# Kernel tuning notes

Measured on AMD Instinct MI355X. Metric: run time of the kernel, lower is better.

## Reference

```python
import jax, jax.numpy as jnp
import numpy as np

EPS = 1e-12  # tf.math.l2_normalize default epsilon

def _l2_normalize(x, axis):
    sq = jnp.sum(x * x, axis=axis, keepdims=True)
    return x * jax.lax.rsqrt(jnp.maximum(sq, EPS))

def setup_inputs() -> dict:
    key = jax.random.key(0)
    k1, k2 = jax.random.split(key)
    B, L, D, K = 4096, 200, 64, 8
    inputs = jax.random.normal(k1, (B, L, D), dtype=jnp.float32)
    prototype = jax.random.normal(k2, (K, D), dtype=jnp.float32)
    return {"inputs": inputs, "prototype": prototype}

def reference(inputs, prototype):
    # inputs: [B, L, D], prototype: [K, D]
    normed_interests = _l2_normalize(inputs, axis=-1)      # [B, L, D]
    normed_prototype = _l2_normalize(prototype, axis=-1)   # [K, D]
    # cosine_sim: [B, K, L] = prototype @ interests^T (broadcast over batch)
    cosine_sim = jnp.einsum('kd,bld->bkl', normed_prototype, normed_interests)
    # softmax over the slot/prototype axis K (axis=-2)
    attn = jax.nn.softmax(cosine_sim, axis=-2)              # [B, K, L]
    # projected interests: [B, K, D]
    return jnp.einsum('bkl,bld->bkd', attn, inputs)
```

## Files before the change

### kernel.cpp

```cpp
#include <hip/hip_runtime.h>


#define LQ 200
#define DQ 64
#define KQ 8
#define NSTEP 25

__device__ __forceinline__ float dppx1(float v) {
    return __int_as_float(__builtin_amdgcn_update_dpp(0, __float_as_int(v), 0xB1, 0xF, 0xF, true));
}
__device__ __forceinline__ float dppx2(float v) {
    return __int_as_float(__builtin_amdgcn_update_dpp(0, __float_as_int(v), 0x4E, 0xF, 0xF, true));
}
__device__ __forceinline__ float swz4(float v) {
    return __int_as_float(__builtin_amdgcn_ds_swizzle(__float_as_int(v), 0x101F));
}
__device__ __forceinline__ float allred8(float v) {
    v += dppx1(v); v += dppx2(v); v += swz4(v); return v;
}
__device__ __forceinline__ float dot4f(float4 a, float4 b) {
    return a.x * b.x + a.y * b.y + a.z * b.z + a.w * b.w;
}
__device__ __forceinline__ void fma4(float4& acc, float a, float4 v) {
    acc.x += a * v.x; acc.y += a * v.y; acc.z += a * v.z; acc.w += a * v.w;
}

__device__ __forceinline__ float reduce_dots(const float* s, bool b1, bool b2, bool b3) {
    float T0 = (b1 ? s[1] : s[0]) + dppx1(b1 ? s[0] : s[1]);
    float T1 = (b1 ? s[3] : s[2]) + dppx1(b1 ? s[2] : s[3]);
    float T2 = (b1 ? s[5] : s[4]) + dppx1(b1 ? s[4] : s[5]);
    float T3 = (b1 ? s[7] : s[6]) + dppx1(b1 ? s[6] : s[7]);
    float K0 = (b2 ? T1 : T0) + dppx2(b2 ? T0 : T1);
    float K1 = (b2 ? T3 : T2) + dppx2(b2 ? T2 : T3);
    return (b3 ? K1 : K0) + swz4(b3 ? K0 : K1);
}

__global__ __launch_bounds__(64, 3) void projector_kernel(const float* __restrict__ x,
                                                          const float* __restrict__ proto,
                                                          float* __restrict__ out) {
    __shared__ __align__(16) float xL[8 * DQ];
    __shared__ __align__(16) float aL[8 * KQ];

    const int b = blockIdx.x;
    const int t = threadIdx.x;
    const int c  = t & 7;
    const int r8 = t >> 3;
    const bool b1 = (c & 1) != 0;
    const bool b2 = (c & 2) != 0;
    const bool b3 = (c & 4) != 0;

    const float4* p4  = (const float4*)proto;
    const float4* xb4 = (const float4*)(x + (size_t)b * (LQ * DQ));

    float4 pA[KQ], pB[KQ];
    #pragma unroll
    for (int k = 0; k < KQ; ++k) {
        pA[k] = p4[k * 16 + 2 * c];
        pB[k] = p4[k * 16 + 2 * c + 1];
    }
    float rnp;
    {
        float sp[KQ];
        #pragma unroll
        for (int k = 0; k < KQ; ++k) sp[k] = dot4f(pA[k], pA[k]) + dot4f(pB[k], pB[k]);
        rnp = __builtin_amdgcn_rsqf(fmaxf(reduce_dots(sp, b1, b2, b3), 1e-12f));
    }

    float4 acc0 = make_float4(0.f, 0.f, 0.f, 0.f), acc1 = acc0;

    float4 xA = xb4[r8 * 16 + 2 * c], xB = xb4[r8 * 16 + 2 * c + 1];

    #pragma unroll 1
    for (int it = 0; it < NSTEP; ++it) {
        const int nr = (it + 1 < NSTEP ? (it + 1) * 8 : (NSTEP - 1) * 8) + r8;
        float4 nA = xb4[nr * 16 + 2 * c];
        float4 nB = xb4[nr * 16 + 2 * c + 1];

        float s[KQ];
        #pragma unroll
        for (int k = 0; k < KQ; ++k)
            s[k] = dot4f(xA, pA[k]) + dot4f(xB, pB[k]);
        float d  = reduce_dots(s, b1, b2, b3) * rnp;
        float sq = allred8(dot4f(xA, xA) + dot4f(xB, xB));
        float e  = __expf(d * __builtin_amdgcn_rsqf(fmaxf(sq, 1e-12f)));
        float a  = e * __builtin_amdgcn_rcpf(allred8(e));

        ((float4*)xL)[r8 * 16 + 2 * c]     = xA;
        ((float4*)xL)[r8 * 16 + 2 * c + 1] = xB;
        aL[t] = a;

        #pragma unroll
        for (int r = 0; r < 8; ++r) {
            float  av  = aL[r * KQ + r8];
            float4 xv0 = ((const float4*)xL)[r * 16 + 2 * c];
            float4 xv1 = ((const float4*)xL)[r * 16 + 2 * c + 1];
            fma4(acc0, av, xv0);
            fma4(acc1, av, xv1);
        }

        xA = nA; xB = nB;
    }

    float4* og = (float4*)(out + (size_t)b * (KQ * DQ));
    og[r8 * 16 + 2 * c]     = acc0;
    og[r8 * 16 + 2 * c + 1] = acc1;
}

extern "C" void kernel_launch(void* const* d_in, const int* in_sizes, int n_in,
                              void* d_out, int out_size, void* d_ws, size_t ws_size,
                              hipStream_t stream) {
    const float* x     = (const float*)d_in[0];
    const float* proto = (const float*)d_in[1];
    float* out = (float*)d_out;

    const int Bn = in_sizes[0] / (LQ * DQ);

    projector_kernel<<<Bn, 64, 0, stream>>>(x, proto, out);
}
```

Baseline: 43.94 us.

## Keep per-prototype accumulators in registers and reduce across rows with shuffles

Removes the per-iteration LDS staging of x rows and attention weights. Each thread now broadcasts the 8 softmax numerators within its octet via DPP/swizzle and accumulates all K prototypes for its own row slice in 64 registers. A butterfly shuffle reduction across row groups at the end assembles the outputs. Packed v2f FMAs are used for the dot products. This trades LDS traffic and barriers for much higher register pressure, and the occupancy hint in launch bounds is dropped.

```diff
diff --git a/kernel.cpp b/kernel.cpp
--- a/kernel.cpp
+++ b/kernel.cpp
@@ -5,6 +5,8 @@
 #define DQ 64
 #define KQ 8
 #define NSTEP 25
+
+typedef float v2f __attribute__((ext_vector_type(2)));
 
 __device__ __forceinline__ float dppx1(float v) {
     return __int_as_float(__builtin_amdgcn_update_dpp(0, __float_as_int(v), 0xB1, 0xF, 0xF, true));
@@ -18,12 +20,10 @@
 __device__ __forceinline__ float allred8(float v) {
     v += dppx1(v); v += dppx2(v); v += swz4(v); return v;
 }
-__device__ __forceinline__ float dot4f(float4 a, float4 b) {
-    return a.x * b.x + a.y * b.y + a.z * b.z + a.w * b.w;
+__device__ __forceinline__ v2f fma2(v2f a, v2f b, v2f c) {
+    return __builtin_elementwise_fma(a, b, c);
 }
-__device__ __forceinline__ void fma4(float4& acc, float a, float4 v) {
-    acc.x += a * v.x; acc.y += a * v.y; acc.z += a * v.z; acc.w += a * v.w;
-}
+__device__ __forceinline__ float hsum2(v2f v) { return v.x + v.y; }
 
 __device__ __forceinline__ float reduce_dots(const float* s, bool b1, bool b2, bool b3) {
     float T0 = (b1 ? s[1] : s[0]) + dppx1(b1 ? s[0] : s[1]);
@@ -35,16 +35,13 @@
     return (b3 ? K1 : K0) + swz4(b3 ? K0 : K1);
 }
 
-__global__ __launch_bounds__(64, 3) void projector_kernel(const float* __restrict__ x,
-                                                          const float* __restrict__ proto,
-                                                          float* __restrict__ out) {
-    __shared__ __align__(16) float xL[8 * DQ];
-    __shared__ __align__(16) float aL[8 * KQ];
-
+__global__ __launch_bounds__(64) void projector_kernel(const float* __restrict__ x,
+                                                       const float* __restrict__ proto,
+                                                       float* __restrict__ out) {
     const int b = blockIdx.x;
     const int t = threadIdx.x;
-    const int c  = t & 7;
-    const int r8 = t >> 3;
+    const int c = t & 7;
+    const int a = t >> 3;
     const bool b1 = (c & 1) != 0;
     const bool b2 = (c & 2) != 0;
     const bool b3 = (c & 4) != 0;
@@ -62,48 +59,100 @@
     {
         float sp[KQ];
         #pragma unroll
-        for (int k = 0; k < KQ; ++k) sp[k] = dot4f(pA[k], pA[k]) + dot4f(pB[k], pB[k]);
+        for (int k = 0; k < KQ; ++k) {
+            v2f a0 = {pA[k].x, pA[k].y}, a1 = {pA[k].z, pA[k].w};
+            v2f b0 = {pB[k].x, pB[k].y}, b1v = {pB[k].z, pB[k].w};
+            v2f t2 = fma2(b1v, b1v, fma2(b0, b0, fma2(a1, a1, a0 * a0)));
+            sp[k] = hsum2(t2);
+        }
         rnp = __builtin_amdgcn_rsqf(fmaxf(reduce_dots(sp, b1, b2, b3), 1e-12f));
     }
 
-    float4 acc0 = make_float4(0.f, 0.f, 0.f, 0.f), acc1 = acc0;
+    v2f acc[KQ][4];
+    #pragma unroll
+    for (int j = 0; j < KQ; ++j)
+        #pragma unroll
+        for (int q = 0; q < 4; ++q) acc[j][q] = (v2f){0.f, 0.f};
 
-    float4 xA = xb4[r8 * 16 + 2 * c], xB = xb4[r8 * 16 + 2 * c + 1];
+    float4 f0 = xb4[a * 16 + 2 * c], f1 = xb4[a * 16 + 2 * c + 1];
 
     #pragma unroll 1
     for (int it = 0; it < NSTEP; ++it) {
-        const int nr = (it + 1 < NSTEP ? (it + 1) * 8 : (NSTEP - 1) * 8) + r8;
-        float4 nA = xb4[nr * 16 + 2 * c];
-        float4 nB = xb4[nr * 16 + 2 * c + 1];
+        const int nrow = (it + 1 < NSTEP ? (it + 1) * 8 : (NSTEP - 1) * 8) + a;
+        float4 nf0 = xb4[nrow * 16 + 2 * c];
+        float4 nf1 = xb4[nrow * 16 + 2 * c + 1];
+
+        v2f x0 = {f0.x, f0.y}, x1 = {f0.z, f0.w};
+        v2f x2 = {f1.x, f1.y}, x3 = {f1.z, f1.w};
 
         float s[KQ];
         #pragma unroll
-        for (int k = 0; k < KQ; ++k)
-            s[k] = dot4f(xA, pA[k]) + dot4f(xB, pB[k]);
-        float d  = reduce_dots(s, b1, b2, b3) * rnp;
-        float sq = allred8(dot4f(xA, xA) + dot4f(xB, xB));
-        float e  = __expf(d * __builtin_amdgcn_rsqf(fmaxf(sq, 1e-12f)));
-        float a  = e * __builtin_amdgcn_rcpf(allred8(e));
+        for (int k = 0; k < KQ; ++k) {
+            v2f pa0 = {pA[k].x, pA[k].y}, pa1 = {pA[k].z, pA[k].w};
+            v2f pb0 = {pB[k].x, pB[k].y}, pb1 = {pB[k].z, pB[k].w};
+            v2f t2 = fma2(x3, pb1, fma2(x2, pb0, fma2(x1, pa1, x0 * pa0)));
+            s[k] = hsum2(t2);
+        }
+        float d = reduce_dots(s, b1, b2, b3) * rnp;
 
-        ((float4*)xL)[r8 * 16 + 2 * c]     = xA;
-        ((float4*)xL)[r8 * 16 + 2 * c + 1] = xB;
-        aL[t] = a;
+        v2f q2 = fma2(x3, x3, fma2(x2, x2, fma2(x1, x1, x0 * x0)));
+        float sq = allred8(hsum2(q2));
+
+        float e0 = __expf(d * __builtin_amdgcn_rsqf(fmaxf(sq, 1e-12f)));
+        float e1 = dppx1(e0);
+        float e2 = dppx2(e0);
+        float e3 = dppx2(e1);
+        float e4 = swz4(e0);
+        float e5 = swz4(e1);
+        float e6 = swz4(e2);
+        float e7 = swz4(e3);
+        float rd = __builtin_amdgcn_rcpf(((e0 + e1) + (e2 + e3)) + ((e4 + e5) + (e6 + e7)));
+        float aj[KQ] = {e0 * rd, e1 * rd, e2 * rd, e3 * rd,
+                        e4 * rd, e5 * rd, e6 * rd, e7 * rd};
 
         #pragma unroll
-        for (int r = 0; r < 8; ++r) {
-            float  av  = aL[r * KQ + r8];
-            float4 xv0 = ((const float4*)xL)[r * 16 + 2 * c];
-            float4 xv1 = ((const float4*)xL)[r * 16 + 2 * c + 1];
-            fma4(acc0, av, xv0);
-            fma4(acc1, av, xv1);
+        for (int j = 0; j < KQ; ++j) {
+            v2f aa = {aj[j], aj[j]};
+            acc[j][0] = fma2(aa, x0, acc[j][0]);
+            acc[j][1] = fma2(aa, x1, acc[j][1]);
+            acc[j][2] = fma2(aa, x2, acc[j][2]);
+            acc[j][3] = fma2(aa, x3, acc[j][3]);
         }
 
-        xA = nA; xB = nB;
+        f0 = nf0; f1 = nf1;
     }
 
+    #pragma unroll
+    for (int i = 0; i < 4; ++i)
+        #pragma unroll
+        for (int q = 0; q < 4; ++q) {
+            v2f send = (a & 1) ? acc[i][q] : acc[i + 4][q];
+            v2f keep = (a & 1) ? acc[i + 4][q] : acc[i][q];
+            v2f r = {__shfl_xor(send.x, 8, 64), __shfl_xor(send.y, 8, 64)};
+            acc[i][q] = keep + r;
+        }
+    #pragma unroll
+    for (int i = 0; i < 2; ++i)
+        #pragma unroll
+        for (int q = 0; q < 4; ++q) {
+            v2f send = (a & 2) ? acc[i][q] : acc[i + 2][q];
+            v2f keep = (a & 2) ? acc[i + 2][q] : acc[i][q];
+            v2f r = {__shfl_xor(send.x, 16, 64), __shfl_xor(send.y, 16, 64)};
+            acc[i][q] = keep + r;
+        }
+    #pragma unroll
+    for (int q = 0; q < 4; ++q) {
+        v2f send = (a & 4) ? acc[0][q] : acc[1][q];
+        v2f keep = (a & 4) ? acc[1][q] : acc[0][q];
+        v2f r = {__shfl_xor(send.x, 32, 64), __shfl_xor(send.y, 32, 64)};
+        acc[0][q] = keep + r;
+    }
+
+    const int j = ((a & 1) << 2) | (a & 2) | ((a & 4) >> 2);
+    const int k = c ^ j;
     float4* og = (float4*)(out + (size_t)b * (KQ * DQ));
-    og[r8 * 16 + 2 * c]     = acc0;
-    og[r8 * 16 + 2 * c + 1] = acc1;
+    og[k * 16 + 2 * c]     = make_float4(acc[0][0].x, acc[0][0].y, acc[0][1].x, acc[0][1].y);
+    og[k * 16 + 2 * c + 1] = make_float4(acc[0][2].x, acc[0][2].y, acc[0][3].x, acc[0][3].y);
 }
 
 extern "C" void kernel_launch(void* const* d_in, const int* in_sizes, int n_in,
```

Result: no change. 44.38 us (+1.0%).
